# Optimization experiments

Measured on AMD Instinct MI355X. Metric: run time of the kernel, lower is better.

## Reference

```python
import jax, jax.numpy as jnp
import numpy as np

K = 3          # kernel size
STRIDE = 1
PAD = 1
GROUPS = 32    # GroupNorm groups
EPS = 1e-5


def setup_inputs() -> dict:
    key = jax.random.key(0)
    ks = jax.random.split(key, 6)
    B, Cin, H, W, Cout = 4, 256, 64, 64, 256
    K2 = K * K
    x = jax.random.normal(ks[0], (B, Cin, H, W), jnp.float32)
    offset = jax.random.normal(ks[1], (B, 2 * K2, H, W), jnp.float32)
    mask = jax.random.uniform(ks[2], (B, K2, H, W), jnp.float32)
    weight = jax.random.normal(ks[3], (Cout, Cin, K, K), jnp.float32) * (1.0 / np.sqrt(Cin * K2))
    bias = jnp.zeros((Cout,), jnp.float32)
    gamma = jnp.ones((Cout,), jnp.float32)   # constant_init(norm, 1)
    beta = jnp.zeros((Cout,), jnp.float32)   # bias=0
    return {"x": x, "offset": offset, "mask": mask, "weight": weight,
            "bias": bias, "gamma": gamma, "beta": beta}


def _modulated_deform_conv(x, offset, mask, weight, bias):
    """DCNv2: bilinear-sample x at learned offsets, modulate by mask, conv-accumulate."""
    B, Cin, H, W = x.shape
    Cout = weight.shape[0]
    K2 = K * K
    Ho = (H + 2 * PAD - K) // STRIDE + 1
    Wo = (W + 2 * PAD - K) // STRIDE + 1

    # base sampling grid per kernel point: [K2, Ho, Wo]
    ky, kx = jnp.meshgrid(jnp.arange(K), jnp.arange(K), indexing='ij')
    ky = ky.reshape(K2).astype(jnp.float32)
    kx = kx.reshape(K2).astype(jnp.float32)
    hs = (jnp.arange(Ho) * STRIDE - PAD).astype(jnp.float32)
    ws = (jnp.arange(Wo) * STRIDE - PAD).astype(jnp.float32)

    off = offset.reshape(B, K2, 2, Ho, Wo)  # interleaved (dy, dx) per kernel point
    y = ky[None, :, None, None] + hs[None, None, :, None] + off[:, :, 0]   # [B,K2,Ho,Wo]
    xc = kx[None, :, None, None] + ws[None, None, None, :] + off[:, :, 1]  # [B,K2,Ho,Wo]

    y0 = jnp.floor(y)
    x0 = jnp.floor(xc)
    dy = y - y0
    dx = xc - x0
    y0i = y0.astype(jnp.int32)
    x0i = x0.astype(jnp.int32)

    x_flat = x.reshape(B, Cin, H * W)

    def corner(yi, xi, w):
        # corner-wise zero padding outside the image (matches mmcv bilinear)
        valid = (yi >= 0) & (yi <= H - 1) & (xi >= 0) & (xi <= W - 1)
        idx = jnp.clip(yi, 0, H - 1) * W + jnp.clip(xi, 0, W - 1)  # [B,K2,Ho,Wo]
        idx_f = idx.reshape(B, -1)
        v = jax.vmap(lambda xf, i: xf[:, i])(x_flat, idx_f)  # [B, Cin, K2*Ho*Wo]
        wv = (w * valid.astype(w.dtype)).reshape(B, 1, -1)
        return v * wv

    val = (corner(y0i,     x0i,     (1 - dy) * (1 - dx))
         + corner(y0i,     x0i + 1, (1 - dy) * dx)
         + corner(y0i + 1, x0i,     dy * (1 - dx))
         + corner(y0i + 1, x0i + 1, dy * dx))
    val = val.reshape(B, Cin, K2, Ho, Wo) * mask[:, None]  # modulate

    w_r = weight.reshape(Cout, Cin, K2)
    out = jnp.einsum('bckhw,ock->bohw', val, w_r) + bias[None, :, None, None]
    return out


def _group_norm(x, gamma, beta):
    B, C, H, W = x.shape
    g = x.reshape(B, GROUPS, C // GROUPS, H, W)
    mu = g.mean(axis=(2, 3, 4), keepdims=True)
    var = ((g - mu) ** 2).mean(axis=(2, 3, 4), keepdims=True)
    g = (g - mu) * jax.lax.rsqrt(var + EPS)
    return g.reshape(B, C, H, W) * gamma[None, :, None, None] + beta[None, :, None, None]


def reference(x, offset, mask, weight, bias, gamma, beta):
    out = _modulated_deform_conv(x, offset, mask, weight, bias)
    out = _group_norm(out, gamma, beta)
    return jax.nn.relu(out)
```

## Files before the change

### kernel.cpp

```cpp
#include <hip/hip_runtime.h>
#include <math.h>

#define BB    4
#define CIN   256
#define HH    64
#define WWID  64
#define COUT  256
#define KKS   3
#define K2    9
#define PADV  1
#define HWSZ  4096
#define GROUPS 32
#define CPG   8
#define EPSV  1e-5f
#define KTOT  2304
#define ROWB  4608
#define NTOT  16384
#define NCHUNK 18

typedef __attribute__((ext_vector_type(8))) short bf16x8;
typedef __attribute__((ext_vector_type(4))) float f32x4;

#define GLOAD_LDS16(g, l) \
    __builtin_amdgcn_global_load_lds((const __attribute__((address_space(1))) unsigned int*)(g), \
                                     (__attribute__((address_space(3))) unsigned int*)(l), 16, 0, 0)

__device__ __forceinline__ unsigned short f2bf(float f) {
    unsigned u = __float_as_uint(f);
    u = (u + 0x7fffu + ((u >> 16) & 1u)) >> 16;
    return (unsigned short)u;
}
__device__ __forceinline__ float bflo(unsigned q) { return __uint_as_float(q << 16); }
__device__ __forceinline__ float bfhi(unsigned q) { return __uint_as_float(q & 0xffff0000u); }

__device__ __forceinline__ int physchunk(int c, int row) {
    return ((c & 7) ^ (row & 7)) | ((c & 8) ^ ((row & 1) << 3));
}

__device__ __forceinline__ void fma8(float* f, float w, uint4 q) {
    f[0] += w * bflo(q.x); f[1] += w * bfhi(q.x);
    f[2] += w * bflo(q.y); f[3] += w * bfhi(q.y);
    f[4] += w * bflo(q.z); f[5] += w * bfhi(q.z);
    f[6] += w * bflo(q.w); f[7] += w * bfhi(q.w);
}

__global__ __launch_bounds__(256)
void k_pre(const float* __restrict__ x, unsigned short* __restrict__ xh,
           const float* __restrict__ w, unsigned short* __restrict__ wtb,
           float* __restrict__ gstat) {
    int t = threadIdx.x;
    if (blockIdx.x < 128) {
        __shared__ float tile[32][33];
        int hw0 = blockIdx.x * 32;
        int c0  = blockIdx.y * 32;
        int b   = blockIdx.z;
        int tx = t & 31, ty = t >> 5;
        const float* xp = x + (size_t)b * CIN * HWSZ;
        #pragma unroll
        for (int i = 0; i < 4; i++)
            tile[ty + i * 8][tx] = xp[(c0 + ty + i * 8) * HWSZ + hw0 + tx];
        __syncthreads();
        int j = t >> 3, cq = t & 7;
        union { unsigned short s[4]; uint2 d; } pk;
        #pragma unroll
        for (int k = 0; k < 4; k++) pk.s[k] = f2bf(tile[cq * 4 + k][j]);
        *(uint2*)((char*)xh + ((size_t)b * HWSZ * CIN + (size_t)(hw0 + j) * CIN + c0 + cq * 4) * 2) = pk.d;
    } else {
        if (blockIdx.y == 0 && blockIdx.z == 0 && t < BB * GROUPS * 2) gstat[t] = 0.f;
        int idx = (blockIdx.y * 4 + blockIdx.z) * 256 + t;
        int co = idx >> 5, c8 = idx & 31;
        int cin0 = c8 * 8;
        int w2 = c8 >> 4, c = c8 & 15;
        int pc = physchunk(c, co);
        for (int k2 = 0; k2 < K2; k2++) {
            union { unsigned short s[8]; uint4 q; } pk;
            #pragma unroll
            for (int j = 0; j < 8; j++)
                pk.s[j] = f2bf(w[(co * CIN + cin0 + j) * K2 + k2]);
            int phys = co * ROWB + k2 * 512 + w2 * 256 + pc * 16;
            *(uint4*)((char*)wtb + phys) = pk.q;
        }
    }
}

__global__ __launch_bounds__(256)
void k_gemm(const unsigned short* __restrict__ wtb, const unsigned short* __restrict__ xh,
            const float* __restrict__ offset, const float* __restrict__ mask,
            const float* __restrict__ bias, float* __restrict__ out,
            float* __restrict__ gstat) {
    __shared__ unsigned short As[128 * 128];
    __shared__ unsigned short Bs[64 * 128];
    __shared__ int   cidx[64 * K2 * 4];
    __shared__ float cwgt[64 * K2 * 4];
    __shared__ float gs[16], gss[16];

    int m0 = blockIdx.x * 128, n0 = blockIdx.y * 64;
    int b = n0 >> 12;
    int t = threadIdx.x, w = t >> 6, l = t & 63;
    int r16 = l & 15, half = l >> 4;
    int wm = w & 1, wn = w >> 1;

    if (t < 16) { gs[t] = 0.f; gss[t] = 0.f; }

    for (int i = t; i < 64 * K2; i += 256) {
        int px = i / K2, k2 = i - px * K2;
        int hw = (n0 & 4095) + px;
        int ho = hw >> 6, wo = hw & 63;
        int ky = k2 / KKS, kx = k2 - ky * KKS;
        float dy = offset[((b * (2 * K2) + k2 * 2 + 0) * HWSZ) + hw];
        float dx = offset[((b * (2 * K2) + k2 * 2 + 1) * HWSZ) + hw];
        float m  = mask[(b * K2 + k2) * HWSZ + hw];
        float y  = (float)(ky + ho - PADV) + dy;
        float xc = (float)(kx + wo - PADV) + dx;
        float y0f = floorf(y), x0f = floorf(xc);
        float fy = y - y0f, fx = xc - x0f;
        int y0 = (int)y0f, x0 = (int)x0f;
        int   yy[2] = { y0, y0 + 1 };
        int   xx[2] = { x0, x0 + 1 };
        float wy[2] = { 1.f - fy, fy };
        float wx[2] = { 1.f - fx, fx };
        #pragma unroll
        for (int ii = 0; ii < 2; ii++)
            #pragma unroll
            for (int jj = 0; jj < 2; jj++) {
                int yi = yy[ii], xi = xx[jj];
                bool valid = (yi >= 0) && (yi < HH) && (xi >= 0) && (xi < WWID);
                int yc  = min(max(yi, 0), HH - 1);
                int xcc = min(max(xi, 0), WWID - 1);
                cidx[i * 4 + ii * 2 + jj] = yc * WWID + xcc;
                cwgt[i * 4 + ii * 2 + jj] = valid ? (wy[ii] * wx[jj] * m) : 0.f;
            }
    }

    const char* ag[8]; unsigned short* lA[8];
    #pragma unroll
    for (int i = 0; i < 8; i++) {
        int o = (w * 8 + i) * 64 + l;
        ag[i] = (const char*)wtb + (size_t)(m0 + (o >> 4)) * ROWB + (o & 15) * 16;
        lA[i] = (unsigned short*)As + (w * 8 + i) * 512;
    }

    int sc  = t & 15;
    int tpx = t >> 4;
    const char* xb = (const char*)xh + (size_t)b * HWSZ * CIN * 2;

    f32x4 acc[4][2];
    #pragma unroll
    for (int mi = 0; mi < 4; mi++)
        #pragma unroll
        for (int ni = 0; ni < 2; ni++) acc[mi][ni] = (f32x4)0.f;

    __syncthreads();

    for (int kc = 0; kc < NCHUNK; kc++) {
        #pragma unroll
        for (int i = 0; i < 8; i++) { GLOAD_LDS16(ag[i], lA[i]); ag[i] += 256; }

        int k2 = kc >> 1, h = kc & 1;
        const char* xbs = xb + h * 256 + sc * 16;
        uint4 g[4][4];
        #pragma unroll
        for (int ps = 0; ps < 4; ps++) {
            int cb = ((ps * 16 + tpx) * K2 + k2) * 4;
            #pragma unroll
            for (int c = 0; c < 4; c++)
                g[ps][c] = *(const uint4*)(xbs + (size_t)cidx[cb + c] * 512);
        }
        #pragma unroll
        for (int ps = 0; ps < 4; ps++) {
            int px = ps * 16 + tpx;
            int cb = (px * K2 + k2) * 4;
            float f[8] = {0,0,0,0,0,0,0,0};
            fma8(f, cwgt[cb + 0], g[ps][0]);
            fma8(f, cwgt[cb + 1], g[ps][1]);
            fma8(f, cwgt[cb + 2], g[ps][2]);
            fma8(f, cwgt[cb + 3], g[ps][3]);
            union { unsigned short s[8]; uint4 q; } pk;
            #pragma unroll
            for (int e = 0; e < 8; e++) pk.s[e] = f2bf(f[e]);
            *(uint4*)&Bs[px * 128 + physchunk(sc, px) * 8] = pk.q;
        }
        __syncthreads();

        #pragma unroll
        for (int ks = 0; ks < 4; ks++) {
            int ks4 = ks * 4 + half;
            int up  = physchunk(ks4, r16) * 8;
            bf16x8 af[4], bfv[2];
            #pragma unroll
            for (int mi = 0; mi < 4; mi++)
                af[mi] = *(const bf16x8*)&As[(wm * 64 + mi * 16 + r16) * 128 + up];
            #pragma unroll
            for (int ni = 0; ni < 2; ni++)
                bfv[ni] = *(const bf16x8*)&Bs[(wn * 32 + ni * 16 + r16) * 128 + up];
            #pragma unroll
            for (int mi = 0; mi < 4; mi++)
                #pragma unroll
                for (int ni = 0; ni < 2; ni++)
                    acc[mi][ni] = __builtin_amdgcn_mfma_f32_16x16x32_bf16(
                        af[mi], bfv[ni], acc[mi][ni], 0, 0, 0);
        }
        __syncthreads();
    }

    float s4[4] = {0,0,0,0}, ss4[4] = {0,0,0,0};
    #pragma unroll
    for (int mi = 0; mi < 4; mi++) {
        #pragma unroll
        for (int r = 0; r < 4; r++) {
            int co = m0 + wm * 64 + mi * 16 + half * 4 + r;
            float bs = bias[co];
            float* orow = out + ((size_t)(b * COUT + co)) * HWSZ;
            #pragma unroll
            for (int ni = 0; ni < 2; ni++) {
                int n = (n0 + wn * 32 + ni * 16 + r16) & 4095;
                float v = acc[mi][ni][r] + bs;
                orow[n] = v;
                s4[mi] += v; ss4[mi] += v * v;
            }
        }
    }
    int gb = half >> 1;
    #pragma unroll
    for (int mi = 0; mi < 4; mi++) {
        atomicAdd(&gs [wm * 8 + mi * 2 + gb], s4[mi]);
        atomicAdd(&gss[wm * 8 + mi * 2 + gb], ss4[mi]);
    }
    __syncthreads();
    if (t < 16) {
        int g = blockIdx.x * 16 + t;
        atomicAdd(&gstat[((b * GROUPS) + g) * 2 + 0], gs[t]);
        atomicAdd(&gstat[((b * GROUPS) + g) * 2 + 1], gss[t]);
    }
}

__global__ __launch_bounds__(256)
void k_gnfinal(float* __restrict__ out, const float* __restrict__ gstat,
               const float* __restrict__ gamma, const float* __restrict__ beta) {
    int i4 = blockIdx.x * 256 + threadIdx.x;
    int e  = i4 * 4;
    int c  = (e >> 12) & 255;
    int b  = e >> 20;
    int g  = c >> 3;
    float s  = gstat[((b * GROUPS) + g) * 2 + 0];
    float ss = gstat[((b * GROUPS) + g) * 2 + 1];
    const float inv = 1.f / (float)(CPG * HWSZ);
    float mu  = s * inv;
    float var = ss * inv - mu * mu;
    float rstd = rsqrtf(var + EPSV);
    float ga = gamma[c] * rstd;
    float be = beta[c] - mu * ga;
    float4 v = ((float4*)out)[i4];
    v.x = fmaxf(v.x * ga + be, 0.f);
    v.y = fmaxf(v.y * ga + be, 0.f);
    v.z = fmaxf(v.z * ga + be, 0.f);
    v.w = fmaxf(v.w * ga + be, 0.f);
    ((float4*)out)[i4] = v;
}

extern "C" void kernel_launch(void* const* d_in, const int* in_sizes, int n_in,
                              void* d_out, int out_size, void* d_ws, size_t ws_size,
                              hipStream_t stream) {
    const float* x      = (const float*)d_in[0];
    const float* offset = (const float*)d_in[1];
    const float* mask   = (const float*)d_in[2];
    const float* weight = (const float*)d_in[3];
    const float* bias   = (const float*)d_in[4];
    const float* gamma  = (const float*)d_in[5];
    const float* beta   = (const float*)d_in[6];
    float* out = (float*)d_out;

    unsigned short* xh    = (unsigned short*)d_ws;
    unsigned short* wtb   = xh + (size_t)4194304;
    float*          gstat = (float*)(wtb + (size_t)589824);

    k_pre<<<dim3(129, 8, 4), 256, 0, stream>>>(x, xh, weight, wtb, gstat);
    k_gemm<<<dim3(2, 256), 256, 0, stream>>>(wtb, xh, offset, mask, bias, out, gstat);
    k_gnfinal<<<(size_t)BB * COUT * HWSZ / 1024, 256, 0, stream>>>(out, gstat, gamma, beta);
}
```

Before: 162.2 us.

## Fuse deform-conv GEMM and GroupNorm into one cooperative kernel with grid barrier

Merges the GEMM and the GroupNorm finalize kernels into a single cooperative kernel. Each block now computes all 256 output channels for a 64-pixel strip, keeps the results in registers, waits at a global atomic barrier until the group statistics are complete, then normalizes and writes the output once. This removes the extra read and write of the output tensor and one launch. The K loop is also reworked into 36 double-buffered chunks of 64, prefetching the next gather and weight tile while the MFMAs run, and the swizzle layout is simplified to match. The cost is a spin barrier whose correctness depends on all 256 blocks being co-resident at 512 threads each.

```diff
diff --git a/kernel.cpp b/kernel.cpp
--- a/kernel.cpp
+++ b/kernel.cpp
@@ -13,10 +13,8 @@
 #define GROUPS 32
 #define CPG   8
 #define EPSV  1e-5f
-#define KTOT  2304
 #define ROWB  4608
-#define NTOT  16384
-#define NCHUNK 18
+#define NKC   36
 
 typedef __attribute__((ext_vector_type(8))) short bf16x8;
 typedef __attribute__((ext_vector_type(4))) float f32x4;
@@ -32,11 +30,9 @@
 }
 __device__ __forceinline__ float bflo(unsigned q) { return __uint_as_float(q << 16); }
 __device__ __forceinline__ float bfhi(unsigned q) { return __uint_as_float(q & 0xffff0000u); }
-
-__device__ __forceinline__ int physchunk(int c, int row) {
-    return ((c & 7) ^ (row & 7)) | ((c & 8) ^ ((row & 1) << 3));
-}
-
+__device__ __forceinline__ float aload(const float* p) {
+    return __hip_atomic_load(p, __ATOMIC_RELAXED, __HIP_MEMORY_SCOPE_AGENT);
+}
 __device__ __forceinline__ void fma8(float* f, float w, uint4 q) {
     f[0] += w * bflo(q.x); f[1] += w * bfhi(q.x);
     f[2] += w * bflo(q.y); f[3] += w * bfhi(q.y);
@@ -66,45 +62,51 @@
         for (int k = 0; k < 4; k++) pk.s[k] = f2bf(tile[cq * 4 + k][j]);
         *(uint2*)((char*)xh + ((size_t)b * HWSZ * CIN + (size_t)(hw0 + j) * CIN + c0 + cq * 4) * 2) = pk.d;
     } else {
-        if (blockIdx.y == 0 && blockIdx.z == 0 && t < BB * GROUPS * 2) gstat[t] = 0.f;
+        if (blockIdx.y == 0 && blockIdx.z == 0)
+            for (int i = t; i < BB * GROUPS * 2 + 8; i += 256) gstat[i] = 0.f;
         int idx = (blockIdx.y * 4 + blockIdx.z) * 256 + t;
         int co = idx >> 5, c8 = idx & 31;
         int cin0 = c8 * 8;
-        int w2 = c8 >> 4, c = c8 & 15;
-        int pc = physchunk(c, co);
+        int q = c8 >> 3, c = c8 & 7;
+        int pc = c ^ (co & 7);
         for (int k2 = 0; k2 < K2; k2++) {
-            union { unsigned short s[8]; uint4 q; } pk;
+            union { unsigned short s[8]; uint4 qq; } pk;
             #pragma unroll
             for (int j = 0; j < 8; j++)
                 pk.s[j] = f2bf(w[(co * CIN + cin0 + j) * K2 + k2]);
-            int phys = co * ROWB + k2 * 512 + w2 * 256 + pc * 16;
-            *(uint4*)((char*)wtb + phys) = pk.q;
-        }
-    }
-}
-
-__global__ __launch_bounds__(256)
-void k_gemm(const unsigned short* __restrict__ wtb, const unsigned short* __restrict__ xh,
+            int phys = co * ROWB + k2 * 512 + q * 128 + pc * 16;
+            *(uint4*)((char*)wtb + phys) = pk.qq;
+        }
+    }
+}
+
+__global__ __launch_bounds__(512, 2)
+void k_mega(const unsigned short* __restrict__ wtb, const unsigned short* __restrict__ xh,
             const float* __restrict__ offset, const float* __restrict__ mask,
-            const float* __restrict__ bias, float* __restrict__ out,
-            float* __restrict__ gstat) {
-    __shared__ unsigned short As[128 * 128];
-    __shared__ unsigned short Bs[64 * 128];
+            const float* __restrict__ bias, const float* __restrict__ gamma,
+            const float* __restrict__ beta, float* __restrict__ out,
+            float* __restrict__ gstat, int* __restrict__ cnt) {
+    __shared__ unsigned short As[2][256 * 64];
+    __shared__ unsigned short Bs[2][64 * 64];
     __shared__ int   cidx[64 * K2 * 4];
     __shared__ float cwgt[64 * K2 * 4];
-    __shared__ float gs[16], gss[16];
-
-    int m0 = blockIdx.x * 128, n0 = blockIdx.y * 64;
-    int b = n0 >> 12;
-    int t = threadIdx.x, w = t >> 6, l = t & 63;
+    __shared__ float gs[32], gss[32], gmu[32], grstd[32];
+
+    int bid = blockIdx.x;
+    int strip = ((bid & 7) << 5) | (bid >> 3);
+    int b = strip >> 6;
+    int hwbase = (strip & 63) * 64;
+    int t = threadIdx.x;
+    int w = t >> 6, l = t & 63;
     int r16 = l & 15, half = l >> 4;
-    int wm = w & 1, wn = w >> 1;
-
-    if (t < 16) { gs[t] = 0.f; gss[t] = 0.f; }
-
-    for (int i = t; i < 64 * K2; i += 256) {
+    int wm = w & 3, wn = w >> 2;
+    int gb = half >> 1;
+
+    if (t < 32) { gs[t] = 0.f; gss[t] = 0.f; }
+
+    for (int i = t; i < 64 * K2; i += 512) {
         int px = i / K2, k2 = i - px * K2;
-        int hw = (n0 & 4095) + px;
+        int hw = hwbase + px;
         int ho = hw >> 6, wo = hw & 63;
         int ky = k2 / KKS, kx = k2 - ky * KKS;
         float dy = offset[((b * (2 * K2) + k2 * 2 + 0) * HWSZ) + hw];
@@ -132,17 +134,17 @@
             }
     }
 
-    const char* ag[8]; unsigned short* lA[8];
-    #pragma unroll
-    for (int i = 0; i < 8; i++) {
-        int o = (w * 8 + i) * 64 + l;
-        ag[i] = (const char*)wtb + (size_t)(m0 + (o >> 4)) * ROWB + (o & 15) * 16;
-        lA[i] = (unsigned short*)As + (w * 8 + i) * 512;
-    }
-
-    int sc  = t & 15;
-    int tpx = t >> 4;
+    const char* ag[4]; int lo[4];
+    #pragma unroll
+    for (int i = 0; i < 4; i++) {
+        int o = i * 512 + t;
+        ag[i] = (const char*)wtb + (size_t)(o >> 3) * ROWB + (o & 7) * 16;
+        lo[i] = o * 8;
+    }
+
+    int spx = t >> 3, sc = t & 7;
     const char* xb = (const char*)xh + (size_t)b * HWSZ * CIN * 2;
+    int bofs = spx * 64 + (sc ^ (spx & 7)) * 8;
 
     f32x4 acc[4][2];
     #pragma unroll
@@ -152,55 +154,66 @@
 
     __syncthreads();
 
-    for (int kc = 0; kc < NCHUNK; kc++) {
-        #pragma unroll
-        for (int i = 0; i < 8; i++) { GLOAD_LDS16(ag[i], lA[i]); ag[i] += 256; }
-
-        int k2 = kc >> 1, h = kc & 1;
-        const char* xbs = xb + h * 256 + sc * 16;
-        uint4 g[4][4];
-        #pragma unroll
-        for (int ps = 0; ps < 4; ps++) {
-            int cb = ((ps * 16 + tpx) * K2 + k2) * 4;
-            #pragma unroll
-            for (int c = 0; c < 4; c++)
-                g[ps][c] = *(const uint4*)(xbs + (size_t)cidx[cb + c] * 512);
-        }
-        #pragma unroll
-        for (int ps = 0; ps < 4; ps++) {
-            int px = ps * 16 + tpx;
-            int cb = (px * K2 + k2) * 4;
+    uint4 g[4]; float gw[4];
+    {
+        int cb = (spx * K2 + 0) * 4;
+        #pragma unroll
+        for (int c = 0; c < 4; c++) {
+            gw[c] = cwgt[cb + c];
+            g[c]  = *(const uint4*)(xb + (size_t)cidx[cb + c] * 512 + sc * 16);
+        }
+    }
+    #pragma unroll
+    for (int i = 0; i < 4; i++) GLOAD_LDS16(ag[i], &As[0][lo[i]]);
+
+    for (int kc = 0; kc < NKC; kc++) {
+        int cur = kc & 1;
+        {
             float f[8] = {0,0,0,0,0,0,0,0};
-            fma8(f, cwgt[cb + 0], g[ps][0]);
-            fma8(f, cwgt[cb + 1], g[ps][1]);
-            fma8(f, cwgt[cb + 2], g[ps][2]);
-            fma8(f, cwgt[cb + 3], g[ps][3]);
-            union { unsigned short s[8]; uint4 q; } pk;
+            fma8(f, gw[0], g[0]); fma8(f, gw[1], g[1]);
+            fma8(f, gw[2], g[2]); fma8(f, gw[3], g[3]);
+            union { unsigned short s[8]; uint4 qq; } pk;
             #pragma unroll
             for (int e = 0; e < 8; e++) pk.s[e] = f2bf(f[e]);
-            *(uint4*)&Bs[px * 128 + physchunk(sc, px) * 8] = pk.q;
+            *(uint4*)&Bs[cur][bofs] = pk.qq;
         }
         __syncthreads();
 
-        #pragma unroll
-        for (int ks = 0; ks < 4; ks++) {
-            int ks4 = ks * 4 + half;
-            int up  = physchunk(ks4, r16) * 8;
-            bf16x8 af[4], bfv[2];
+        if (kc < NKC - 1) {
+            int kn = kc + 1;
+            int k2n = kn >> 2, qn = kn & 3;
+            int cb = (spx * K2 + k2n) * 4;
+            #pragma unroll
+            for (int c = 0; c < 4; c++) {
+                gw[c] = cwgt[cb + c];
+                g[c]  = *(const uint4*)(xb + (size_t)cidx[cb + c] * 512 + qn * 128 + sc * 16);
+            }
+            #pragma unroll
+            for (int i = 0; i < 4; i++) {
+                ag[i] += 128;
+                GLOAD_LDS16(ag[i], &As[1 - cur][lo[i]]);
+            }
+        }
+
+        const unsigned short* Ap = As[cur];
+        const unsigned short* Bp = Bs[cur];
+        #pragma unroll
+        for (int ks = 0; ks < 2; ks++) {
+            int up = ((ks * 4 + half) ^ (r16 & 7)) * 8;
+            bf16x8 af[4], bv[2];
             #pragma unroll
             for (int mi = 0; mi < 4; mi++)
-                af[mi] = *(const bf16x8*)&As[(wm * 64 + mi * 16 + r16) * 128 + up];
+                af[mi] = *(const bf16x8*)&Ap[(wm * 64 + mi * 16 + r16) * 64 + up];
             #pragma unroll
             for (int ni = 0; ni < 2; ni++)
-                bfv[ni] = *(const bf16x8*)&Bs[(wn * 32 + ni * 16 + r16) * 128 + up];
+                bv[ni] = *(const bf16x8*)&Bp[(wn * 32 + ni * 16 + r16) * 64 + up];
             #pragma unroll
             for (int mi = 0; mi < 4; mi++)
                 #pragma unroll
                 for (int ni = 0; ni < 2; ni++)
                     acc[mi][ni] = __builtin_amdgcn_mfma_f32_16x16x32_bf16(
-                        af[mi], bfv[ni], acc[mi][ni], 0, 0, 0);
-        }
-        __syncthreads();
+                        af[mi], bv[ni], acc[mi][ni], 0, 0, 0);
+        }
     }
 
     float s4[4] = {0,0,0,0}, ss4[4] = {0,0,0,0};
@@ -208,54 +221,62 @@
     for (int mi = 0; mi < 4; mi++) {
         #pragma unroll
         for (int r = 0; r < 4; r++) {
-            int co = m0 + wm * 64 + mi * 16 + half * 4 + r;
-            float bs = bias[co];
-            float* orow = out + ((size_t)(b * COUT + co)) * HWSZ;
+            float bs = bias[wm * 64 + mi * 16 + half * 4 + r];
             #pragma unroll
             for (int ni = 0; ni < 2; ni++) {
-                int n = (n0 + wn * 32 + ni * 16 + r16) & 4095;
                 float v = acc[mi][ni][r] + bs;
-                orow[n] = v;
+                acc[mi][ni][r] = v;
                 s4[mi] += v; ss4[mi] += v * v;
             }
         }
     }
-    int gb = half >> 1;
     #pragma unroll
     for (int mi = 0; mi < 4; mi++) {
         atomicAdd(&gs [wm * 8 + mi * 2 + gb], s4[mi]);
         atomicAdd(&gss[wm * 8 + mi * 2 + gb], ss4[mi]);
     }
     __syncthreads();
-    if (t < 16) {
-        int g = blockIdx.x * 16 + t;
-        atomicAdd(&gstat[((b * GROUPS) + g) * 2 + 0], gs[t]);
-        atomicAdd(&gstat[((b * GROUPS) + g) * 2 + 1], gss[t]);
-    }
-}
-
-__global__ __launch_bounds__(256)
-void k_gnfinal(float* __restrict__ out, const float* __restrict__ gstat,
-               const float* __restrict__ gamma, const float* __restrict__ beta) {
-    int i4 = blockIdx.x * 256 + threadIdx.x;
-    int e  = i4 * 4;
-    int c  = (e >> 12) & 255;
-    int b  = e >> 20;
-    int g  = c >> 3;
-    float s  = gstat[((b * GROUPS) + g) * 2 + 0];
-    float ss = gstat[((b * GROUPS) + g) * 2 + 1];
+    if (t < 32) {
+        atomicAdd(&gstat[(b * GROUPS + t) * 2 + 0], gs[t]);
+        atomicAdd(&gstat[(b * GROUPS + t) * 2 + 1], gss[t]);
+    }
+
+    if (t == 0) {
+        __threadfence();
+        atomicAdd(cnt, 1);
+        while (__hip_atomic_load(cnt, __ATOMIC_ACQUIRE, __HIP_MEMORY_SCOPE_AGENT) < (int)gridDim.x)
+            __builtin_amdgcn_s_sleep(4);
+    }
+    __syncthreads();
+
     const float inv = 1.f / (float)(CPG * HWSZ);
-    float mu  = s * inv;
-    float var = ss * inv - mu * mu;
-    float rstd = rsqrtf(var + EPSV);
-    float ga = gamma[c] * rstd;
-    float be = beta[c] - mu * ga;
-    float4 v = ((float4*)out)[i4];
-    v.x = fmaxf(v.x * ga + be, 0.f);
-    v.y = fmaxf(v.y * ga + be, 0.f);
-    v.z = fmaxf(v.z * ga + be, 0.f);
-    v.w = fmaxf(v.w * ga + be, 0.f);
-    ((float4*)out)[i4] = v;
+    if (t < 32) {
+        float s  = aload(&gstat[(b * GROUPS + t) * 2 + 0]);
+        float ss = aload(&gstat[(b * GROUPS + t) * 2 + 1]);
+        float mu  = s * inv;
+        float var = ss * inv - mu * mu;
+        gmu[t]   = mu;
+        grstd[t] = rsqrtf(var + EPSV);
+    }
+    __syncthreads();
+
+    #pragma unroll
+    for (int mi = 0; mi < 4; mi++) {
+        int gl = wm * 8 + mi * 2 + gb;
+        float mu = gmu[gl], rstd = grstd[gl];
+        #pragma unroll
+        for (int r = 0; r < 4; r++) {
+            int co = wm * 64 + mi * 16 + half * 4 + r;
+            float ga = gamma[co] * rstd;
+            float be = beta[co] - mu * ga;
+            float* orow = out + ((size_t)(b * COUT + co)) * HWSZ;
+            #pragma unroll
+            for (int ni = 0; ni < 2; ni++) {
+                int n = hwbase + wn * 32 + ni * 16 + r16;
+                orow[n] = fmaxf(acc[mi][ni][r] * ga + be, 0.f);
+            }
+        }
+    }
 }
 
 extern "C" void kernel_launch(void* const* d_in, const int* in_sizes, int n_in,
@@ -273,8 +294,13 @@
     unsigned short* xh    = (unsigned short*)d_ws;
     unsigned short* wtb   = xh + (size_t)4194304;
     float*          gstat = (float*)(wtb + (size_t)589824);
+    int*            cnt   = (int*)(gstat + 256);
 
     k_pre<<<dim3(129, 8, 4), 256, 0, stream>>>(x, xh, weight, wtb, gstat);
-    k_gemm<<<dim3(2, 256), 256, 0, stream>>>(wtb, xh, offset, mask, bias, out, gstat);
-    k_gnfinal<<<(size_t)BB * COUT * HWSZ / 1024, 256, 0, stream>>>(out, gstat, gamma, beta);
-}
+
+    const unsigned short* wtb_c = wtb; const unsigned short* xh_c = xh;
+    void* args[] = { (void*)&wtb_c, (void*)&xh_c, (void*)&offset, (void*)&mask,
+                     (void*)&bias, (void*)&gamma, (void*)&beta, (void*)&out,
+                     (void*)&gstat, (void*)&cnt };
+    hipLaunchCooperativeKernel((void*)k_mega, dim3(256), dim3(512), args, 0, stream);
+}
```

Measured after the change: 187.3 us. 1.15x slower.

## Halve K-chunk size and prefetch next chunk's bilinear gathers during MFMA

Applied to the files above, without the earlier changes.

The deformable-conv GEMM now uses 64-wide K chunks (36 iterations) with smaller LDS tiles and a simpler XOR swizzle. The global gathers for the next chunk are issued into registers right after the barrier, so they overlap with the current chunk's MFMA work. Blocks are remapped to a 1D grid that interleaves M tiles and pixel strips, which is meant to improve L2 locality. The cost is twice as many barriers per block and higher register pressure from holding the prefetched data.

```diff
diff --git a/kernel.cpp b/kernel.cpp
--- a/kernel.cpp
+++ b/kernel.cpp
@@ -13,10 +13,8 @@
 #define GROUPS 32
 #define CPG   8
 #define EPSV  1e-5f
-#define KTOT  2304
 #define ROWB  4608
-#define NTOT  16384
-#define NCHUNK 18
+#define NKC   36
 
 typedef __attribute__((ext_vector_type(8))) short bf16x8;
 typedef __attribute__((ext_vector_type(4))) float f32x4;
@@ -32,11 +30,6 @@
 }
 __device__ __forceinline__ float bflo(unsigned q) { return __uint_as_float(q << 16); }
 __device__ __forceinline__ float bfhi(unsigned q) { return __uint_as_float(q & 0xffff0000u); }
-
-__device__ __forceinline__ int physchunk(int c, int row) {
-    return ((c & 7) ^ (row & 7)) | ((c & 8) ^ ((row & 1) << 3));
-}
-
 __device__ __forceinline__ void fma8(float* f, float w, uint4 q) {
     f[0] += w * bflo(q.x); f[1] += w * bfhi(q.x);
     f[2] += w * bflo(q.y); f[3] += w * bfhi(q.y);
@@ -66,45 +59,53 @@
         for (int k = 0; k < 4; k++) pk.s[k] = f2bf(tile[cq * 4 + k][j]);
         *(uint2*)((char*)xh + ((size_t)b * HWSZ * CIN + (size_t)(hw0 + j) * CIN + c0 + cq * 4) * 2) = pk.d;
     } else {
-        if (blockIdx.y == 0 && blockIdx.z == 0 && t < BB * GROUPS * 2) gstat[t] = 0.f;
+        if (blockIdx.y == 0 && blockIdx.z == 0)
+            for (int i = t; i < BB * GROUPS * 2 + 8; i += 256) gstat[i] = 0.f;
         int idx = (blockIdx.y * 4 + blockIdx.z) * 256 + t;
         int co = idx >> 5, c8 = idx & 31;
         int cin0 = c8 * 8;
-        int w2 = c8 >> 4, c = c8 & 15;
-        int pc = physchunk(c, co);
+        int q = c8 >> 3, c = c8 & 7;
+        int pc = c ^ (co & 7);
         for (int k2 = 0; k2 < K2; k2++) {
-            union { unsigned short s[8]; uint4 q; } pk;
+            union { unsigned short s[8]; uint4 qq; } pk;
             #pragma unroll
             for (int j = 0; j < 8; j++)
                 pk.s[j] = f2bf(w[(co * CIN + cin0 + j) * K2 + k2]);
-            int phys = co * ROWB + k2 * 512 + w2 * 256 + pc * 16;
-            *(uint4*)((char*)wtb + phys) = pk.q;
+            int phys = co * ROWB + k2 * 512 + q * 128 + pc * 16;
+            *(uint4*)((char*)wtb + phys) = pk.qq;
         }
     }
 }
 
 __global__ __launch_bounds__(256)
-void k_gemm(const unsigned short* __restrict__ wtb, const unsigned short* __restrict__ xh,
+void k_conv(const unsigned short* __restrict__ wtb, const unsigned short* __restrict__ xh,
             const float* __restrict__ offset, const float* __restrict__ mask,
             const float* __restrict__ bias, float* __restrict__ out,
             float* __restrict__ gstat) {
-    __shared__ unsigned short As[128 * 128];
-    __shared__ unsigned short Bs[64 * 128];
+    __shared__ unsigned short As[128 * 64];
+    __shared__ unsigned short Bs[64 * 64];
     __shared__ int   cidx[64 * K2 * 4];
     __shared__ float cwgt[64 * K2 * 4];
     __shared__ float gs[16], gss[16];
 
-    int m0 = blockIdx.x * 128, n0 = blockIdx.y * 64;
-    int b = n0 >> 12;
+    int lid = blockIdx.x;
+    int j8  = lid >> 3;
+    int mt  = j8 & 1;
+    int strip = (lid & 7) * 32 + (j8 >> 1);
+    int b = strip >> 6;
+    int hwbase = (strip & 63) * 64;
+    int m0 = mt * 128;
+
     int t = threadIdx.x, w = t >> 6, l = t & 63;
     int r16 = l & 15, half = l >> 4;
     int wm = w & 1, wn = w >> 1;
+    int skey = r16 & 7;
 
     if (t < 16) { gs[t] = 0.f; gss[t] = 0.f; }
 
     for (int i = t; i < 64 * K2; i += 256) {
         int px = i / K2, k2 = i - px * K2;
-        int hw = (n0 & 4095) + px;
+        int hw = hwbase + px;
         int ho = hw >> 6, wo = hw & 63;
         int ky = k2 / KKS, kx = k2 - ky * KKS;
         float dy = offset[((b * (2 * K2) + k2 * 2 + 0) * HWSZ) + hw];
@@ -132,17 +133,20 @@
             }
     }
 
-    const char* ag[8]; unsigned short* lA[8];
-    #pragma unroll
-    for (int i = 0; i < 8; i++) {
-        int o = (w * 8 + i) * 64 + l;
-        ag[i] = (const char*)wtb + (size_t)(m0 + (o >> 4)) * ROWB + (o & 15) * 16;
-        lA[i] = (unsigned short*)As + (w * 8 + i) * 512;
-    }
-
-    int sc  = t & 15;
-    int tpx = t >> 4;
+    const char* ag[4]; unsigned short* lA[4];
+    #pragma unroll
+    for (int i = 0; i < 4; i++) {
+        int o = i * 256 + t;
+        ag[i] = (const char*)wtb + (size_t)(m0 + (o >> 3)) * ROWB + (o & 7) * 16;
+        lA[i] = (unsigned short*)As + o * 8;
+    }
+
+    int sc  = t & 7;
+    int px0 = t >> 3;
     const char* xb = (const char*)xh + (size_t)b * HWSZ * CIN * 2;
+    int bofs0 = px0 * 64 + (sc ^ (px0 & 7)) * 8;
+    int px1 = px0 + 32;
+    int bofs1 = px1 * 64 + (sc ^ (px1 & 7)) * 8;
 
     f32x4 acc[4][2];
     #pragma unroll
@@ -152,53 +156,63 @@
 
     __syncthreads();
 
-    for (int kc = 0; kc < NCHUNK; kc++) {
-        #pragma unroll
-        for (int i = 0; i < 8; i++) { GLOAD_LDS16(ag[i], lA[i]); ag[i] += 256; }
-
-        int k2 = kc >> 1, h = kc & 1;
-        const char* xbs = xb + h * 256 + sc * 16;
-        uint4 g[4][4];
-        #pragma unroll
-        for (int ps = 0; ps < 4; ps++) {
-            int cb = ((ps * 16 + tpx) * K2 + k2) * 4;
-            #pragma unroll
-            for (int c = 0; c < 4; c++)
-                g[ps][c] = *(const uint4*)(xbs + (size_t)cidx[cb + c] * 512);
-        }
-        #pragma unroll
-        for (int ps = 0; ps < 4; ps++) {
-            int px = ps * 16 + tpx;
-            int cb = (px * K2 + k2) * 4;
+    uint4 g[2][4]; float gw[2][4];
+    #pragma unroll
+    for (int it = 0; it < 2; it++) {
+        int cb = ((it ? px1 : px0) * K2) * 4;
+        #pragma unroll
+        for (int c = 0; c < 4; c++) {
+            gw[it][c] = cwgt[cb + c];
+            g[it][c]  = *(const uint4*)(xb + (size_t)cidx[cb + c] * 512 + sc * 16);
+        }
+    }
+
+    for (int kc = 0; kc < NKC; kc++) {
+        #pragma unroll
+        for (int i = 0; i < 4; i++) { GLOAD_LDS16(ag[i], lA[i]); ag[i] += 128; }
+
+        #pragma unroll
+        for (int it = 0; it < 2; it++) {
             float f[8] = {0,0,0,0,0,0,0,0};
-            fma8(f, cwgt[cb + 0], g[ps][0]);
-            fma8(f, cwgt[cb + 1], g[ps][1]);
-            fma8(f, cwgt[cb + 2], g[ps][2]);
-            fma8(f, cwgt[cb + 3], g[ps][3]);
-            union { unsigned short s[8]; uint4 q; } pk;
+            fma8(f, gw[it][0], g[it][0]); fma8(f, gw[it][1], g[it][1]);
+            fma8(f, gw[it][2], g[it][2]); fma8(f, gw[it][3], g[it][3]);
+            union { unsigned short s[8]; uint4 qq; } pk;
             #pragma unroll
             for (int e = 0; e < 8; e++) pk.s[e] = f2bf(f[e]);
-            *(uint4*)&Bs[px * 128 + physchunk(sc, px) * 8] = pk.q;
+            *(uint4*)&Bs[it ? bofs1 : bofs0] = pk.qq;
         }
         __syncthreads();
 
-        #pragma unroll
-        for (int ks = 0; ks < 4; ks++) {
-            int ks4 = ks * 4 + half;
-            int up  = physchunk(ks4, r16) * 8;
-            bf16x8 af[4], bfv[2];
+        if (kc < NKC - 1) {
+            int kn = kc + 1;
+            int k2n = kn >> 2, qn = kn & 3;
+            #pragma unroll
+            for (int it = 0; it < 2; it++) {
+                int cb = ((it ? px1 : px0) * K2 + k2n) * 4;
+                #pragma unroll
+                for (int c = 0; c < 4; c++) {
+                    gw[it][c] = cwgt[cb + c];
+                    g[it][c]  = *(const uint4*)(xb + (size_t)cidx[cb + c] * 512 + qn * 128 + sc * 16);
+                }
+            }
+        }
+
+        #pragma unroll
+        for (int ks = 0; ks < 2; ks++) {
+            int up = ((ks * 4 + half) ^ skey) * 8;
+            bf16x8 af[4], bv[2];
             #pragma unroll
             for (int mi = 0; mi < 4; mi++)
-                af[mi] = *(const bf16x8*)&As[(wm * 64 + mi * 16 + r16) * 128 + up];
+                af[mi] = *(const bf16x8*)&As[(wm * 64 + mi * 16 + r16) * 64 + up];
             #pragma unroll
             for (int ni = 0; ni < 2; ni++)
-                bfv[ni] = *(const bf16x8*)&Bs[(wn * 32 + ni * 16 + r16) * 128 + up];
+                bv[ni] = *(const bf16x8*)&Bs[(wn * 32 + ni * 16 + r16) * 64 + up];
             #pragma unroll
             for (int mi = 0; mi < 4; mi++)
                 #pragma unroll
                 for (int ni = 0; ni < 2; ni++)
                     acc[mi][ni] = __builtin_amdgcn_mfma_f32_16x16x32_bf16(
-                        af[mi], bfv[ni], acc[mi][ni], 0, 0, 0);
+                        af[mi], bv[ni], acc[mi][ni], 0, 0, 0);
         }
         __syncthreads();
     }
@@ -213,7 +227,7 @@
             float* orow = out + ((size_t)(b * COUT + co)) * HWSZ;
             #pragma unroll
             for (int ni = 0; ni < 2; ni++) {
-                int n = (n0 + wn * 32 + ni * 16 + r16) & 4095;
+                int n = hwbase + wn * 32 + ni * 16 + r16;
                 float v = acc[mi][ni][r] + bs;
                 orow[n] = v;
                 s4[mi] += v; ss4[mi] += v * v;
@@ -228,9 +242,9 @@
     }
     __syncthreads();
     if (t < 16) {
-        int g = blockIdx.x * 16 + t;
-        atomicAdd(&gstat[((b * GROUPS) + g) * 2 + 0], gs[t]);
-        atomicAdd(&gstat[((b * GROUPS) + g) * 2 + 1], gss[t]);
+        int gidx = (m0 >> 3) + t;
+        atomicAdd(&gstat[(b * GROUPS + gidx) * 2 + 0], gs[t]);
+        atomicAdd(&gstat[(b * GROUPS + gidx) * 2 + 1], gss[t]);
     }
 }
 
@@ -275,6 +289,6 @@
     float*          gstat = (float*)(wtb + (size_t)589824);
 
     k_pre<<<dim3(129, 8, 4), 256, 0, stream>>>(x, xh, weight, wtb, gstat);
-    k_gemm<<<dim3(2, 256), 256, 0, stream>>>(wtb, xh, offset, mask, bias, out, gstat);
+    k_conv<<<512, 256, 0, stream>>>(wtb, xh, offset, mask, bias, out, gstat);
     k_gnfinal<<<(size_t)BB * COUT * HWSZ / 1024, 256, 0, stream>>>(out, gstat, gamma, beta);
 }
```

After: 151.3 us. 6.7% less time.
